# Kernel optimization log

Hardware: AMD Instinct MI355X
Metric: run time of the kernel (lower is better)

Reference implementation:

```python
import jax, jax.numpy as jnp
import numpy as np

L, H, C, HS, E, K, V, BS = 2, 12, 768, 64, 8, 2, 32000, 1024
B, T = 2, 1024


def layer_norm(x, s, b):
    mu = x.mean(-1, keepdims=True)
    var = ((x - mu) ** 2).mean(-1, keepdims=True)
    return (x - mu) / jnp.sqrt(var + 1e-5) * s + b


def setup_inputs() -> dict:
    key = jax.random.key(0)
    ks = jax.random.split(key, 16)
    def n(k, shape, s=0.02):
        return jax.random.normal(k, shape, dtype=jnp.float32) * s
    return {
        'idx': jax.random.randint(ks[0], (B, T), 0, V),
        'targets': jax.random.randint(ks[1], (B, T), 0, V),
        'tok_emb': n(ks[2], (V, C)),
        'pos_emb': n(ks[3], (BS, C)),
        'ln1_s': jnp.ones((L, C), jnp.float32), 'ln1_b': jnp.zeros((L, C), jnp.float32),
        'wq': n(ks[4], (L, H, C, HS)), 'wk': n(ks[5], (L, H, C, HS)), 'wv': n(ks[6], (L, H, C, HS)),
        'wo': n(ks[7], (L, C, C)), 'bo': jnp.zeros((L, C), jnp.float32),
        'ln2_s': jnp.ones((L, C), jnp.float32), 'ln2_b': jnp.zeros((L, C), jnp.float32),
        'gate_w': n(ks[8], (L, E, C)),
        'w1': n(ks[9], (L, E, 4 * C, C)), 'b1': jnp.zeros((L, E, 4 * C), jnp.float32),
        'w2': n(ks[10], (L, E, C, 4 * C)), 'b2': jnp.zeros((L, E, C), jnp.float32),
        'lm_w': n(ks[11], (V, C)), 'lm_b': jnp.zeros((V,), jnp.float32),
    }


def reference(idx, targets, tok_emb, pos_emb, ln1_s, ln1_b, wq, wk, wv, wo, bo,
              ln2_s, ln2_b, gate_w, w1, b1, w2, b2, lm_w, lm_b):
    Bsz, Tn = idx.shape
    x = tok_emb[idx] + pos_emb[:Tn]                       # [B,T,C]
    mask = jnp.tril(jnp.ones((Tn, Tn), bool))
    for l in range(L):
        # causal multi-head attention (per-head projections, scale = n_embed**-0.5 as in source)
        h = layer_norm(x, ln1_s[l], ln1_b[l])
        q = jnp.einsum('btc,hcd->bhtd', h, wq[l])
        k = jnp.einsum('btc,hcd->bhtd', h, wk[l])
        v = jnp.einsum('btc,hcd->bhtd', h, wv[l])
        att = jnp.einsum('bhtd,bhsd->bhts', q, k) * (C ** -0.5)
        att = jax.nn.softmax(jnp.where(mask, att, -jnp.inf), axis=-1)
        o = jnp.einsum('bhts,bhsd->bhtd', att, v)
        o = o.transpose(0, 2, 1, 3).reshape(Bsz, Tn, C)   # concat heads
        x = x + jnp.einsum('btc,oc->bto', o, wo[l]) + bo[l]
        # MoE FFN: top-k routing, softmax over selected gate logits
        h2 = layer_norm(x, ln2_s[l], ln2_b[l]).reshape(-1, C)     # [N,C]
        gl = jnp.einsum('tc,ec->te', h2, gate_w[l])               # [N,E]
        wts, sel = jax.lax.top_k(gl, K)
        wts = jax.nn.softmax(wts, axis=-1)
        comb = jnp.einsum('tk,tke->te', wts, jax.nn.one_hot(sel, E, dtype=wts.dtype))
        hid = jax.nn.relu(jnp.einsum('tc,efc->etf', h2, w1[l]) + b1[l][:, None, :])
        y = jnp.einsum('etf,ecf->etc', hid, w2[l]) + b2[l][:, None, :]
        moe = jnp.einsum('te,etc->tc', comb, y)                   # dispatch-weighted combine
        x = x + moe.reshape(Bsz, Tn, C)
    logits = jnp.einsum('btc,vc->btv', x, lm_w) + lm_b
    lf = logits.reshape(-1, V)
    tf = targets.reshape(-1)
    loss = -jnp.take_along_axis(jax.nn.log_softmax(lf, axis=-1), tf[:, None], axis=1).mean()
    return lf, loss
```

## Files before the change

kernel.cpp:

```cpp
#include <hip/hip_runtime.h>
#include <hip/hip_bf16.h>

#define LCNT 2
#define HCNT 12
#define CDIM 768
#define HSD  64
#define ECNT 8
#define VOC  32000
#define BB   2
#define TT   1024
#define NTOK 2048
#define FF   3072
#define QKVLD 2304
#define TOTCAP 5120

typedef __attribute__((ext_vector_type(8))) short bf16x8;
typedef __attribute__((ext_vector_type(4))) float f32x4;

__device__ __forceinline__ float wave_sum(float v) {
    #pragma unroll
    for (int off = 32; off; off >>= 1) v += __shfl_xor(v, off);
    return v;
}
__device__ __forceinline__ float wave_max(float v) {
    #pragma unroll
    for (int off = 32; off; off >>= 1) v = fmaxf(v, __shfl_xor(v, off));
    return v;
}
__device__ __forceinline__ unsigned short f2bf(float f) {
    unsigned int u = __float_as_uint(f);
    unsigned int r = (u + 0x7FFFu + ((u >> 16) & 1u)) >> 16;
    return (unsigned short)r;
}
__device__ __forceinline__ float bf2f(unsigned short h) {
    return __uint_as_float((unsigned int)h << 16);
}
__device__ __forceinline__ void split2(float a, unsigned short& h, unsigned short& l) {
    h = f2bf(a);
    l = f2bf(a - bf2f(h));
}
__device__ __forceinline__ ushort4 cvt4(float4 v) {
    ushort4 r;
    r.x = f2bf(v.x); r.y = f2bf(v.y); r.z = f2bf(v.z); r.w = f2bf(v.w);
    return r;
}

__global__ __launch_bounds__(256)
void embed_kernel(const int* __restrict__ idx, const float* __restrict__ tok,
                  const float* __restrict__ pos, float* __restrict__ x)
{
    int i = blockIdx.x * 256 + threadIdx.x;
    int c = i % CDIM;
    int n = i / CDIM;
    int t = n % TT;
    x[i] = tok[(size_t)idx[n] * CDIM + c] + pos[(size_t)t * CDIM + c];
}

__global__ __launch_bounds__(256)
void repack_kernel(const float* __restrict__ wq, const float* __restrict__ wk,
                   const float* __restrict__ wv, float* __restrict__ wp)
{
    int i = blockIdx.x * 256 + threadIdx.x;
    int kk = i % CDIM;
    int n  = (i / CDIM) % CDIM;
    int w3 = (i / (CDIM * CDIM)) % 3;
    int l  = i / (CDIM * CDIM * 3);
    const float* src = (w3 == 0) ? wq : (w3 == 1) ? wk : wv;
    int h = n / HSD, d = n % HSD;
    wp[(((size_t)l * 3 + w3) * CDIM + n) * CDIM + kk] =
        src[((((size_t)l * HCNT + h) * CDIM) + kk) * HSD + d];
}

__global__ __launch_bounds__(256)
void ln_kernel(const float* __restrict__ x, const float* __restrict__ sc,
               const float* __restrict__ bs, float* __restrict__ out)
{
    int row = blockIdx.x;
    const float* xr = x + (size_t)row * CDIM;
    float* orow = out + (size_t)row * CDIM;
    int tid = threadIdx.x;
    float v0 = xr[tid], v1 = xr[tid + 256], v2 = xr[tid + 512];
    float s1 = v0 + v1 + v2;
    float s2 = v0 * v0 + v1 * v1 + v2 * v2;
    s1 = wave_sum(s1);
    s2 = wave_sum(s2);
    __shared__ float r1[4], r2[4];
    int w = tid >> 6, lane = tid & 63;
    if (lane == 0) { r1[w] = s1; r2[w] = s2; }
    __syncthreads();
    float t1 = r1[0] + r1[1] + r1[2] + r1[3];
    float t2 = r2[0] + r2[1] + r2[2] + r2[3];
    float mu = t1 * (1.0f / CDIM);
    float var = t2 * (1.0f / CDIM) - mu * mu;
    float rstd = rsqrtf(var + 1e-5f);
    orow[tid]       = (v0 - mu) * rstd * sc[tid]       + bs[tid];
    orow[tid + 256] = (v1 - mu) * rstd * sc[tid + 256] + bs[tid + 256];
    orow[tid + 512] = (v2 - mu) * rstd * sc[tid + 512] + bs[tid + 512];
}

#define BM 128
#define BN 128
#define BK 32
#define PADK 40

template<int MODE, bool SPLIT, bool SWZ = false>
__global__ __launch_bounds__(256)
void gemm_bf16_kernel(int Kd,
                      const float* __restrict__ A, int lda,
                      const float* __restrict__ B, int ldb,
                      const float* __restrict__ bias,
                      float* __restrict__ out, int ldo,
                      const int* __restrict__ rowmeta,
                      size_t bstride, int biasstride)
{
    __shared__ short Ah[BM * PADK];
    __shared__ short Bh[BN * PADK];
    __shared__ short Al[SPLIT ? BM * PADK : 2];
    __shared__ short Bl[SPLIT ? BN * PADK : 2];

    int bx = blockIdx.x, by = blockIdx.y;
    if constexpr (SWZ) {
        const int nwg = gridDim.x * gridDim.y;
        const int chunk = nwg >> 3;
        const int flat = by * gridDim.x + bx;
        const int newid = (flat & 7) * chunk + (flat >> 3);
        by = newid % gridDim.y;
        bx = newid / gridDim.y;
    }

    int roff = 0;
    if (rowmeta) {
        const int ee = blockIdx.z;
        const int rcnt = rowmeta[2 * ee + 1];
        if ((int)(by * BM) >= rcnt) return;
        roff = rowmeta[2 * ee];
        B += (size_t)ee * bstride;
        if (bias) bias += (size_t)ee * biasstride;
    }

    const int tid = threadIdx.x;
    const int m0 = roff + by * BM;
    const int n0 = bx * BN;
    const int w = tid >> 6, lane = tid & 63;
    const int wr = w >> 1, wc = w & 1;
    const int lrow = lane & 15, lkg = lane >> 4;
    const int srow = tid >> 3, skg = (tid & 7) * 4;

    const float* Ablk = A + (size_t)m0 * lda;
    const float* Bblk = B + (size_t)n0 * ldb;

    float4 pa[4], pb[4];
    #pragma unroll
    for (int p = 0; p < 4; ++p) {
        pa[p] = *(const float4*)(Ablk + (size_t)(p * 32 + srow) * lda + skg);
        pb[p] = *(const float4*)(Bblk + (size_t)(p * 32 + srow) * ldb + skg);
    }

    f32x4 acc[4][4] = {};
    const int nk = Kd / BK;

    for (int t = 0; t < nk; ++t) {
        __syncthreads();
        #pragma unroll
        for (int p = 0; p < 4; ++p) {
            if constexpr (SPLIT) {
                ushort4 h, l;
                split2(pa[p].x, h.x, l.x); split2(pa[p].y, h.y, l.y);
                split2(pa[p].z, h.z, l.z); split2(pa[p].w, h.w, l.w);
                *(ushort4*)(&Ah[(p * 32 + srow) * PADK + skg]) = h;
                *(ushort4*)(&Al[(p * 32 + srow) * PADK + skg]) = l;
                split2(pb[p].x, h.x, l.x); split2(pb[p].y, h.y, l.y);
                split2(pb[p].z, h.z, l.z); split2(pb[p].w, h.w, l.w);
                *(ushort4*)(&Bh[(p * 32 + srow) * PADK + skg]) = h;
                *(ushort4*)(&Bl[(p * 32 + srow) * PADK + skg]) = l;
            } else {
                *(ushort4*)(&Ah[(p * 32 + srow) * PADK + skg]) = cvt4(pa[p]);
                *(ushort4*)(&Bh[(p * 32 + srow) * PADK + skg]) = cvt4(pb[p]);
            }
        }
        __syncthreads();
        if (t + 1 < nk) {
            const int kb = (t + 1) * BK + skg;
            #pragma unroll
            for (int p = 0; p < 4; ++p) {
                pa[p] = *(const float4*)(Ablk + (size_t)(p * 32 + srow) * lda + kb);
                pb[p] = *(const float4*)(Bblk + (size_t)(p * 32 + srow) * ldb + kb);
            }
        }
        bf16x8 afh[4], afl[4];
        #pragma unroll
        for (int i = 0; i < 4; ++i) {
            afh[i] = *(const bf16x8*)(&Ah[(wr * 64 + i * 16 + lrow) * PADK + lkg * 8]);
            if constexpr (SPLIT)
                afl[i] = *(const bf16x8*)(&Al[(wr * 64 + i * 16 + lrow) * PADK + lkg * 8]);
        }
        #pragma unroll
        for (int j = 0; j < 4; ++j) {
            const bf16x8 bh = *(const bf16x8*)(&Bh[(wc * 64 + j * 16 + lrow) * PADK + lkg * 8]);
            if constexpr (SPLIT) {
                const bf16x8 bl = *(const bf16x8*)(&Bl[(wc * 64 + j * 16 + lrow) * PADK + lkg * 8]);
                #pragma unroll
                for (int i = 0; i < 4; ++i) {
                    acc[i][j] = __builtin_amdgcn_mfma_f32_16x16x32_bf16(afh[i], bh, acc[i][j], 0, 0, 0);
                    acc[i][j] = __builtin_amdgcn_mfma_f32_16x16x32_bf16(afl[i], bh, acc[i][j], 0, 0, 0);
                    acc[i][j] = __builtin_amdgcn_mfma_f32_16x16x32_bf16(afh[i], bl, acc[i][j], 0, 0, 0);
                }
            } else {
                #pragma unroll
                for (int i = 0; i < 4; ++i)
                    acc[i][j] = __builtin_amdgcn_mfma_f32_16x16x32_bf16(afh[i], bh, acc[i][j], 0, 0, 0);
            }
        }
    }

    #pragma unroll
    for (int i = 0; i < 4; ++i) {
        #pragma unroll
        for (int r = 0; r < 4; ++r) {
            const int row = m0 + wr * 64 + i * 16 + lkg * 4 + r;
            #pragma unroll
            for (int j = 0; j < 4; ++j) {
                const int col = n0 + wc * 64 + j * 16 + lrow;
                const float bj = bias ? bias[col] : 0.0f;
                const float vres = acc[i][j][r] + bj;
                float* op = out + (size_t)row * ldo + col;
                if (MODE == 0) *op = vres;
                else if (MODE == 1) *op = *op + vres;
                else *op = fmaxf(vres, 0.0f);
            }
        }
    }
}

#define QBLK 64
#define KVBLK 64

__global__ __launch_bounds__(256)
void attn_mfma_kernel(const float* __restrict__ qkv, float* __restrict__ o)
{
    __shared__ short Kh[2][KVBLK][PADK];
    __shared__ short Kl[2][KVBLK][PADK];
    __shared__ short Vh[2][HSD][PADK];
    __shared__ short Vl[2][HSD][PADK];
    __shared__ short Ph[4][2][16][PADK];
    __shared__ short Pl[4][2][16][PADK];

    const int t0 = blockIdx.x * QBLK;
    const int bh = blockIdx.y;
    const int b = bh / HCNT, hh = bh % HCNT;
    const size_t baseq = (size_t)b * TT * QKVLD + (size_t)hh * HSD;
    const size_t obase = (size_t)b * TT * CDIM + (size_t)hh * HSD;
    const float* q = qkv + baseq;
    const float* k = qkv + baseq + CDIM;
    const float* v = qkv + baseq + 2 * CDIM;
    const int tid = threadIdx.x;
    const int w = tid >> 6, lane = tid & 63;
    const int lrow = lane & 15, lkg = lane >> 4;
    const float sscale = rsqrtf((float)CDIM);

    bf16x8 qh[2], ql[2];
    {
        const float* qr = q + (size_t)(t0 + w * 16 + lrow) * QKVLD;
        #pragma unroll
        for (int ks = 0; ks < 2; ++ks) {
            #pragma unroll
            for (int j = 0; j < 8; ++j) {
                unsigned short h, l;
                split2(qr[ks * 32 + lkg * 8 + j], h, l);
                qh[ks][j] = (short)h;
                ql[ks][j] = (short)l;
            }
        }
    }

    f32x4 oacc[4] = {};
    float m_[4], l_[4];
    #pragma unroll
    for (int rr = 0; rr < 4; ++rr) { m_[rr] = -1e30f; l_[rr] = 0.0f; }

    for (int s0 = 0; s0 <= t0 + QBLK - 1; s0 += KVBLK) {
        __syncthreads();
        {
            const int srow = tid >> 3, skg = (tid & 7) * 4;
            #pragma unroll
            for (int p = 0; p < 2; ++p) {
                const float* krow = k + (size_t)(s0 + p * 32 + srow) * QKVLD;
                #pragma unroll
                for (int ks = 0; ks < 2; ++ks) {
                    float4 a = *(const float4*)(krow + ks * 32 + skg);
                    ushort4 h, l;
                    split2(a.x, h.x, l.x); split2(a.y, h.y, l.y);
                    split2(a.z, h.z, l.z); split2(a.w, h.w, l.w);
                    *(ushort4*)(&Kh[ks][p * 32 + srow][skg]) = h;
                    *(ushort4*)(&Kl[ks][p * 32 + srow][skg]) = l;
                }
            }
            const int key = tid & 63, dg = (tid >> 6) * 16;
            const float* vrow = v + (size_t)(s0 + key) * QKVLD + dg;
            const int kst = key >> 5, ko = key & 31;
            #pragma unroll
            for (int dd = 0; dd < 16; dd += 4) {
                float4 a = *(const float4*)(vrow + dd);
                unsigned short h, l;
                split2(a.x, h, l); Vh[kst][dg + dd + 0][ko] = h; Vl[kst][dg + dd + 0][ko] = l;
                split2(a.y, h, l); Vh[kst][dg + dd + 1][ko] = h; Vl[kst][dg + dd + 1][ko] = l;
                split2(a.z, h, l); Vh[kst][dg + dd + 2][ko] = h; Vl[kst][dg + dd + 2][ko] = l;
                split2(a.w, h, l); Vh[kst][dg + dd + 3][ko] = h; Vl[kst][dg + dd + 3][ko] = l;
            }
        }
        __syncthreads();

        f32x4 sacc[4] = {};
        #pragma unroll
        for (int j = 0; j < 4; ++j) {
            #pragma unroll
            for (int ks = 0; ks < 2; ++ks) {
                const bf16x8 bh = *(const bf16x8*)(&Kh[ks][j * 16 + lrow][lkg * 8]);
                const bf16x8 bl = *(const bf16x8*)(&Kl[ks][j * 16 + lrow][lkg * 8]);
                sacc[j] = __builtin_amdgcn_mfma_f32_16x16x32_bf16(qh[ks], bh, sacc[j], 0, 0, 0);
                sacc[j] = __builtin_amdgcn_mfma_f32_16x16x32_bf16(ql[ks], bh, sacc[j], 0, 0, 0);
                sacc[j] = __builtin_amdgcn_mfma_f32_16x16x32_bf16(qh[ks], bl, sacc[j], 0, 0, 0);
            }
        }

        #pragma unroll
        for (int rr = 0; rr < 4; ++rr) {
            const int qi = t0 + w * 16 + lkg * 4 + rr;
            float pv[4];
            float mx = -1e30f;
            #pragma unroll
            for (int j = 0; j < 4; ++j) {
                float s = sacc[j][rr] * sscale;
                if (s0 + j * 16 + lrow > qi) s = -1e30f;
                pv[j] = s;
                mx = fmaxf(mx, s);
            }
            #pragma unroll
            for (int off = 1; off < 16; off <<= 1) mx = fmaxf(mx, __shfl_xor(mx, off));
            const float mnew = fmaxf(m_[rr], mx);
            const float corr = __expf(m_[rr] - mnew);
            float ps = 0.0f;
            #pragma unroll
            for (int j = 0; j < 4; ++j) { pv[j] = __expf(pv[j] - mnew); ps += pv[j]; }
            #pragma unroll
            for (int off = 1; off < 16; off <<= 1) ps += __shfl_xor(ps, off);
            l_[rr] = l_[rr] * corr + ps;
            m_[rr] = mnew;
            #pragma unroll
            for (int jd = 0; jd < 4; ++jd) oacc[jd][rr] *= corr;
            #pragma unroll
            for (int j = 0; j < 4; ++j) {
                unsigned short h, l;
                split2(pv[j], h, l);
                const int key = j * 16 + lrow;
                Ph[w][key >> 5][lkg * 4 + rr][key & 31] = h;
                Pl[w][key >> 5][lkg * 4 + rr][key & 31] = l;
            }
        }

        #pragma unroll
        for (int ks = 0; ks < 2; ++ks) {
            const bf16x8 ah = *(const bf16x8*)(&Ph[w][ks][lrow][lkg * 8]);
            const bf16x8 al = *(const bf16x8*)(&Pl[w][ks][lrow][lkg * 8]);
            #pragma unroll
            for (int jd = 0; jd < 4; ++jd) {
                const bf16x8 bh = *(const bf16x8*)(&Vh[ks][jd * 16 + lrow][lkg * 8]);
                const bf16x8 bl = *(const bf16x8*)(&Vl[ks][jd * 16 + lrow][lkg * 8]);
                oacc[jd] = __builtin_amdgcn_mfma_f32_16x16x32_bf16(ah, bh, oacc[jd], 0, 0, 0);
                oacc[jd] = __builtin_amdgcn_mfma_f32_16x16x32_bf16(al, bh, oacc[jd], 0, 0, 0);
                oacc[jd] = __builtin_amdgcn_mfma_f32_16x16x32_bf16(ah, bl, oacc[jd], 0, 0, 0);
            }
        }
    }

    #pragma unroll
    for (int rr = 0; rr < 4; ++rr) {
        const int qi = t0 + w * 16 + lkg * 4 + rr;
        const float invl = 1.0f / l_[rr];
        float* orow = o + obase + (size_t)qi * CDIM;
        #pragma unroll
        for (int jd = 0; jd < 4; ++jd)
            orow[jd * 16 + lrow] = oacc[jd][rr] * invl;
    }
}

__global__ __launch_bounds__(256)
void gate_kernel(const float* __restrict__ h2, const float* __restrict__ gw,
                 int2* __restrict__ sel, float2* __restrict__ wts)
{
    __shared__ float gws[ECNT * CDIM];
    int tid = threadIdx.x;
    for (int i = tid; i < ECNT * CDIM; i += 256) gws[i] = gw[i];
    __syncthreads();
    int t = blockIdx.x * 256 + tid;
    const float* hr = h2 + (size_t)t * CDIM;
    float g[ECNT] = {};
    for (int c = 0; c < CDIM; ++c) {
        float hv = hr[c];
        #pragma unroll
        for (int e = 0; e < ECNT; ++e) g[e] = fmaf(hv, gws[e * CDIM + c], g[e]);
    }
    int e0 = 0; float g0 = g[0];
    #pragma unroll
    for (int e = 1; e < ECNT; ++e) if (g[e] > g0) { g0 = g[e]; e0 = e; }
    int e1 = -1; float g1 = -1e30f;
    #pragma unroll
    for (int e = 0; e < ECNT; ++e) if (e != e0 && g[e] > g1) { g1 = g[e]; e1 = e; }
    float z = __expf(g1 - g0);
    float w0 = 1.0f / (1.0f + z);
    sel[t] = make_int2(e0, e1);
    wts[t] = make_float2(w0, 1.0f - w0);
}

__global__ __launch_bounds__(256)
void route_kernel(const int2* __restrict__ sel, int* __restrict__ perm,
                  int* __restrict__ tokpos, int* __restrict__ meta)
{
    __shared__ int cnt[ECNT], off[ECNT], cur[ECNT];
    const int tid = threadIdx.x;
    if (tid < ECNT) cnt[tid] = 0;
    __syncthreads();
    for (int t = tid; t < NTOK; t += 256) {
        atomicAdd(&cnt[sel[t].x], 1);
        atomicAdd(&cnt[sel[t].y], 1);
    }
    __syncthreads();
    if (tid == 0) {
        int run = 0;
        for (int e = 0; e < ECNT; ++e) {
            off[e] = run; cur[e] = 0;
            int pc = (cnt[e] + BM - 1) / BM * BM;
            meta[2 * e] = run; meta[2 * e + 1] = pc;
            run += pc;
        }
    }
    __syncthreads();
    for (int p = tid; p < TOTCAP; p += 256) perm[p] = 0;
    __syncthreads();
    for (int t = tid; t < NTOK; t += 256) {
        int2 s = sel[t];
        int p0 = atomicAdd(&cur[s.x], 1); perm[off[s.x] + p0] = t; tokpos[2 * t]     = off[s.x] + p0;
        int p1 = atomicAdd(&cur[s.y], 1); perm[off[s.y] + p1] = t; tokpos[2 * t + 1] = off[s.y] + p1;
    }
}

__global__ __launch_bounds__(256)
void gather_kernel(const float* __restrict__ h2, const int* __restrict__ perm,
                   float* __restrict__ xg)
{
    int i = blockIdx.x * 256 + threadIdx.x;
    int c = i % CDIM, p = i / CDIM;
    xg[i] = h2[(size_t)perm[p] * CDIM + c];
}

__global__ __launch_bounds__(256)
void combine_kernel(const float* __restrict__ y, const int* __restrict__ tokpos,
                    const float2* __restrict__ wts, float* __restrict__ x)
{
    int i = blockIdx.x * 256 + threadIdx.x;
    int c = i % CDIM, t = i / CDIM;
    float2 wv = wts[t];
    x[i] += wv.x * y[(size_t)tokpos[2 * t] * CDIM + c]
          + wv.y * y[(size_t)tokpos[2 * t + 1] * CDIM + c];
}

__global__ __launch_bounds__(256)
void loss_row_kernel(const float* __restrict__ logits, const int* __restrict__ tgt,
                     float* __restrict__ lrow)
{
    int row = blockIdx.x;
    const float* lr = logits + (size_t)row * VOC;
    int tid = threadIdx.x, w = tid >> 6, lane = tid & 63;
    __shared__ float red[4];
    float mx = -1e30f;
    for (int i = tid; i < VOC; i += 256) mx = fmaxf(mx, lr[i]);
    mx = wave_max(mx);
    if (lane == 0) red[w] = mx;
    __syncthreads();
    mx = fmaxf(fmaxf(red[0], red[1]), fmaxf(red[2], red[3]));
    __syncthreads();
    float se = 0.0f;
    for (int i = tid; i < VOC; i += 256) se += expf(lr[i] - mx);
    se = wave_sum(se);
    if (lane == 0) red[w] = se;
    __syncthreads();
    if (tid == 0) {
        float lse = mx + logf(red[0] + red[1] + red[2] + red[3]);
        lrow[row] = lse - lr[tgt[row]];
    }
}

__global__ __launch_bounds__(256)
void loss_reduce_kernel(const float* __restrict__ lrow, float* __restrict__ out)
{
    int tid = threadIdx.x, w = tid >> 6, lane = tid & 63;
    float s = 0.0f;
    for (int i = tid; i < NTOK; i += 256) s += lrow[i];
    s = wave_sum(s);
    __shared__ float red[4];
    if (lane == 0) red[w] = s;
    __syncthreads();
    if (tid == 0) out[0] = (red[0] + red[1] + red[2] + red[3]) * (1.0f / NTOK);
}

extern "C" void kernel_launch(void* const* d_in, const int* in_sizes, int n_in,
                              void* d_out, int out_size, void* d_ws, size_t ws_size,
                              hipStream_t stream)
{
    const int*   idx     = (const int*)d_in[0];
    const int*   targets = (const int*)d_in[1];
    const float* tok_emb = (const float*)d_in[2];
    const float* pos_emb = (const float*)d_in[3];
    const float* ln1_s   = (const float*)d_in[4];
    const float* ln1_b   = (const float*)d_in[5];
    const float* wq      = (const float*)d_in[6];
    const float* wk      = (const float*)d_in[7];
    const float* wv      = (const float*)d_in[8];
    const float* wo      = (const float*)d_in[9];
    const float* bo      = (const float*)d_in[10];
    const float* ln2_s   = (const float*)d_in[11];
    const float* ln2_b   = (const float*)d_in[12];
    const float* gate_w  = (const float*)d_in[13];
    const float* w1      = (const float*)d_in[14];
    const float* b1      = (const float*)d_in[15];
    const float* w2      = (const float*)d_in[16];
    const float* b2      = (const float*)d_in[17];
    const float* lm_w    = (const float*)d_in[18];
    const float* lm_b    = (const float*)d_in[19];
    float* out = (float*)d_out;

    float* ws   = (float*)d_ws;
    float* wp   = ws;
    float* x    = wp   + (size_t)3 * LCNT * CDIM * CDIM;
    float* hbuf = x    + (size_t)NTOK * CDIM;
    float* qkv  = hbuf + (size_t)NTOK * CDIM;
    float* xg   = qkv  + (size_t)NTOK * QKVLD;
    float* hid  = xg   + (size_t)TOTCAP * CDIM;
    float* lrow = hid  + (size_t)TOTCAP * FF;
    float2* wts = (float2*)(lrow + NTOK);
    int2*  sel  = (int2*)(wts + NTOK);
    int*   perm = (int*)(sel + NTOK);
    int*  tokpos= perm + TOTCAP;
    int*   meta = tokpos + 2 * NTOK;

    dim3 blk(256);

    repack_kernel<<<(3 * LCNT * CDIM * CDIM) / 256, blk, 0, stream>>>(wq, wk, wv, wp);
    embed_kernel<<<(NTOK * CDIM) / 256, blk, 0, stream>>>(idx, tok_emb, pos_emb, x);

    for (int l = 0; l < LCNT; ++l) {
        ln_kernel<<<NTOK, blk, 0, stream>>>(x, ln1_s + (size_t)l * CDIM, ln1_b + (size_t)l * CDIM, hbuf);

        gemm_bf16_kernel<0, true><<<dim3(QKVLD / BN, NTOK / BM), blk, 0, stream>>>(
            CDIM, hbuf, CDIM, wp + (size_t)l * 3 * CDIM * CDIM, CDIM,
            nullptr, qkv, QKVLD, nullptr, 0, 0);

        attn_mfma_kernel<<<dim3(TT / QBLK, BB * HCNT), blk, 0, stream>>>(qkv, hbuf);

        gemm_bf16_kernel<1, true><<<dim3(CDIM / BN, NTOK / BM), blk, 0, stream>>>(
            CDIM, hbuf, CDIM, wo + (size_t)l * CDIM * CDIM, CDIM,
            bo + (size_t)l * CDIM, x, CDIM, nullptr, 0, 0);

        float* h2 = qkv;
        float* ybuf = qkv;
        ln_kernel<<<NTOK, blk, 0, stream>>>(x, ln2_s + (size_t)l * CDIM, ln2_b + (size_t)l * CDIM, h2);
        gate_kernel<<<NTOK / 256, blk, 0, stream>>>(h2, gate_w + (size_t)l * ECNT * CDIM, sel, wts);
        route_kernel<<<1, blk, 0, stream>>>(sel, perm, tokpos, meta);
        gather_kernel<<<(TOTCAP * CDIM) / 256, blk, 0, stream>>>(h2, perm, xg);

        const float* w1l = w1 + (size_t)l * ECNT * FF * CDIM;
        const float* b1l = b1 + (size_t)l * ECNT * FF;
        const float* w2l = w2 + (size_t)l * ECNT * CDIM * FF;
        const float* b2l = b2 + (size_t)l * ECNT * CDIM;
        if (l == 0) {
            gemm_bf16_kernel<2, true><<<dim3(FF / BN, NTOK / BM, ECNT), blk, 0, stream>>>(
                CDIM, xg, CDIM, w1l, CDIM, b1l, hid, FF, meta, (size_t)FF * CDIM, FF);
            gemm_bf16_kernel<0, true><<<dim3(CDIM / BN, NTOK / BM, ECNT), blk, 0, stream>>>(
                FF, hid, FF, w2l, FF, b2l, ybuf, CDIM, meta, (size_t)CDIM * FF, CDIM);
        } else {
            gemm_bf16_kernel<2, false><<<dim3(FF / BN, NTOK / BM, ECNT), blk, 0, stream>>>(
                CDIM, xg, CDIM, w1l, CDIM, b1l, hid, FF, meta, (size_t)FF * CDIM, FF);
            gemm_bf16_kernel<0, false><<<dim3(CDIM / BN, NTOK / BM, ECNT), blk, 0, stream>>>(
                FF, hid, FF, w2l, FF, b2l, ybuf, CDIM, meta, (size_t)CDIM * FF, CDIM);
        }
        combine_kernel<<<(NTOK * CDIM) / 256, blk, 0, stream>>>(ybuf, tokpos, wts, x);
    }

    gemm_bf16_kernel<0, false, true><<<dim3(VOC / BN, NTOK / BM), blk, 0, stream>>>(
        CDIM, x, CDIM, lm_w, CDIM, lm_b, out, VOC, nullptr, 0, 0);

    loss_row_kernel<<<NTOK, blk, 0, stream>>>(out, targets, lrow);
    loss_reduce_kernel<<<1, blk, 0, stream>>>(lrow, out + (size_t)NTOK * VOC);
}
```

Baseline: 1.508 ms.

## Use bf16 activations and pre-converted weights for layer-1 MoE and LM-head GEMMs

Adds a GEMM variant that reads bf16 A operands, optionally bf16 B, and can write bf16 output. The second-layer MoE FFN now gathers directly into bf16 and stores the hidden activations as bf16. The LM head first converts lm_w and x to bf16 in separate kernels so the GEMM loads half the bytes. The MoE grid's y dimension grows from NTOK/BM to TOTCAP/BM so that experts receiving more than 2048 tokens are fully covered. This cuts memory traffic and in-loop conversions, at the cost of extra conversion passes over the 32000x768 weight every call and lower precision in the intermediates.

Measured after the change: 1.437 ms. -4.7%, faster.

```diff
diff --git a/kernel.cpp b/kernel.cpp
--- a/kernel.cpp
+++ b/kernel.cpp
@@ -46,6 +46,15 @@
 }
 
 __global__ __launch_bounds__(256)
+void cvt_bf16_kernel(const float* __restrict__ in, unsigned short* __restrict__ out, int n4)
+{
+    for (int i = blockIdx.x * 256 + threadIdx.x; i < n4; i += gridDim.x * 256) {
+        float4 v = reinterpret_cast<const float4*>(in)[i];
+        reinterpret_cast<ushort4*>(out)[i] = cvt4(v);
+    }
+}
+
+__global__ __launch_bounds__(256)
 void embed_kernel(const int* __restrict__ idx, const float* __restrict__ tok,
                   const float* __restrict__ pos, float* __restrict__ x)
 {
@@ -103,7 +112,7 @@
 #define BK 32
 #define PADK 40
 
-template<int MODE, bool SPLIT, bool SWZ = false>
+template<int MODE, bool SPLIT>
 __global__ __launch_bounds__(256)
 void gemm_bf16_kernel(int Kd,
                       const float* __restrict__ A, int lda,
@@ -118,29 +127,19 @@
     __shared__ short Al[SPLIT ? BM * PADK : 2];
     __shared__ short Bl[SPLIT ? BN * PADK : 2];
 
-    int bx = blockIdx.x, by = blockIdx.y;
-    if constexpr (SWZ) {
-        const int nwg = gridDim.x * gridDim.y;
-        const int chunk = nwg >> 3;
-        const int flat = by * gridDim.x + bx;
-        const int newid = (flat & 7) * chunk + (flat >> 3);
-        by = newid % gridDim.y;
-        bx = newid / gridDim.y;
-    }
-
     int roff = 0;
     if (rowmeta) {
         const int ee = blockIdx.z;
         const int rcnt = rowmeta[2 * ee + 1];
-        if ((int)(by * BM) >= rcnt) return;
+        if ((int)(blockIdx.y * BM) >= rcnt) return;
         roff = rowmeta[2 * ee];
         B += (size_t)ee * bstride;
         if (bias) bias += (size_t)ee * biasstride;
     }
 
     const int tid = threadIdx.x;
-    const int m0 = roff + by * BM;
-    const int n0 = bx * BN;
+    const int m0 = roff + blockIdx.y * BM;
+    const int n0 = blockIdx.x * BN;
     const int w = tid >> 6, lane = tid & 63;
     const int wr = w >> 1, wc = w & 1;
     const int lrow = lane & 15, lkg = lane >> 4;
@@ -232,6 +231,117 @@
     }
 }
 
+template<int MODE, bool SWZ, bool OUTBF, bool BBF>
+__global__ __launch_bounds__(256)
+void gemm_fastw_kernel(int Kd,
+                       const unsigned short* __restrict__ A, int lda,
+                       const void* __restrict__ Bv, int ldb,
+                       const float* __restrict__ bias,
+                       void* __restrict__ outv, int ldo,
+                       const int* __restrict__ rowmeta,
+                       size_t bstride, int biasstride)
+{
+    __shared__ short Ah[BM * PADK];
+    __shared__ short Bh[BN * PADK];
+
+    int bx = blockIdx.x, by = blockIdx.y;
+    if constexpr (SWZ) {
+        const int nwg = gridDim.x * gridDim.y;
+        const int chunk = nwg >> 3;
+        const int flat = by * gridDim.x + bx;
+        const int newid = (flat & 7) * chunk + (flat >> 3);
+        by = newid % gridDim.y;
+        bx = newid / gridDim.y;
+    }
+
+    const float* Bf = (const float*)Bv;
+    const unsigned short* Bb = (const unsigned short*)Bv;
+    float* outf = (float*)outv;
+    unsigned short* outb = (unsigned short*)outv;
+
+    int roff = 0;
+    if (rowmeta) {
+        const int ee = blockIdx.z;
+        const int rcnt = rowmeta[2 * ee + 1];
+        if ((int)(by * BM) >= rcnt) return;
+        roff = rowmeta[2 * ee];
+        if (BBF) Bb += (size_t)ee * bstride; else Bf += (size_t)ee * bstride;
+        if (bias) bias += (size_t)ee * biasstride;
+    }
+
+    const int tid = threadIdx.x;
+    const int m0 = roff + by * BM;
+    const int n0 = bx * BN;
+    const int w = tid >> 6, lane = tid & 63;
+    const int wr = w >> 1, wc = w & 1;
+    const int lrow = lane & 15, lkg = lane >> 4;
+    const int srow = tid >> 3, skg = (tid & 7) * 4;
+
+    const unsigned short* Ablk = A + (size_t)m0 * lda;
+    const float* Bfblk = Bf + (size_t)n0 * ldb;
+    const unsigned short* Bbblk = Bb + (size_t)n0 * ldb;
+
+    ushort4 pa[4];
+    ushort4 pbb[4];
+    float4  pbf[4];
+    #pragma unroll
+    for (int p = 0; p < 4; ++p) {
+        pa[p] = *(const ushort4*)(Ablk + (size_t)(p * 32 + srow) * lda + skg);
+        if constexpr (BBF) pbb[p] = *(const ushort4*)(Bbblk + (size_t)(p * 32 + srow) * ldb + skg);
+        else               pbf[p] = *(const float4*)(Bfblk + (size_t)(p * 32 + srow) * ldb + skg);
+    }
+
+    f32x4 acc[4][4] = {};
+    const int nk = Kd / BK;
+
+    for (int t = 0; t < nk; ++t) {
+        __syncthreads();
+        #pragma unroll
+        for (int p = 0; p < 4; ++p) {
+            *(ushort4*)(&Ah[(p * 32 + srow) * PADK + skg]) = pa[p];
+            *(ushort4*)(&Bh[(p * 32 + srow) * PADK + skg]) = BBF ? pbb[p] : cvt4(pbf[p]);
+        }
+        __syncthreads();
+        if (t + 1 < nk) {
+            const int kb = (t + 1) * BK + skg;
+            #pragma unroll
+            for (int p = 0; p < 4; ++p) {
+                pa[p] = *(const ushort4*)(Ablk + (size_t)(p * 32 + srow) * lda + kb);
+                if constexpr (BBF) pbb[p] = *(const ushort4*)(Bbblk + (size_t)(p * 32 + srow) * ldb + kb);
+                else               pbf[p] = *(const float4*)(Bfblk + (size_t)(p * 32 + srow) * ldb + kb);
+            }
+        }
+        bf16x8 af[4];
+        #pragma unroll
+        for (int i = 0; i < 4; ++i)
+            af[i] = *(const bf16x8*)(&Ah[(wr * 64 + i * 16 + lrow) * PADK + lkg * 8]);
+        #pragma unroll
+        for (int j = 0; j < 4; ++j) {
+            const bf16x8 bh = *(const bf16x8*)(&Bh[(wc * 64 + j * 16 + lrow) * PADK + lkg * 8]);
+            #pragma unroll
+            for (int i = 0; i < 4; ++i)
+                acc[i][j] = __builtin_amdgcn_mfma_f32_16x16x32_bf16(af[i], bh, acc[i][j], 0, 0, 0);
+        }
+    }
+
+    #pragma unroll
+    for (int i = 0; i < 4; ++i) {
+        #pragma unroll
+        for (int r = 0; r < 4; ++r) {
+            const int row = m0 + wr * 64 + i * 16 + lkg * 4 + r;
+            #pragma unroll
+            for (int j = 0; j < 4; ++j) {
+                const int col = n0 + wc * 64 + j * 16 + lrow;
+                const float bj = bias ? bias[col] : 0.0f;
+                float vres = acc[i][j][r] + bj;
+                if (MODE == 2) vres = fmaxf(vres, 0.0f);
+                if constexpr (OUTBF) outb[(size_t)row * ldo + col] = f2bf(vres);
+                else                 outf[(size_t)row * ldo + col] = vres;
+            }
+        }
+    }
+}
+
 #define QBLK 64
 #define KVBLK 64
 
@@ -451,6 +561,15 @@
     int i = blockIdx.x * 256 + threadIdx.x;
     int c = i % CDIM, p = i / CDIM;
     xg[i] = h2[(size_t)perm[p] * CDIM + c];
+}
+
+__global__ __launch_bounds__(256)
+void gather_bf16_kernel(const float* __restrict__ h2, const int* __restrict__ perm,
+                        unsigned short* __restrict__ xg)
+{
+    int i = blockIdx.x * 256 + threadIdx.x;
+    int c = i % CDIM, p = i / CDIM;
+    xg[i] = f2bf(h2[(size_t)perm[p] * CDIM + c]);
 }
 
 __global__ __launch_bounds__(256)
@@ -542,6 +661,11 @@
     int*   perm = (int*)(sel + NTOK);
     int*  tokpos= perm + TOTCAP;
     int*   meta = tokpos + 2 * NTOK;
+    unsigned short* x_bf = (unsigned short*)(meta + 16);
+
+    unsigned short* xg_bf  = (unsigned short*)xg;
+    unsigned short* hid_bf = (unsigned short*)hid;
+    unsigned short* lmw_bf = (unsigned short*)hid;
 
     dim3 blk(256);
 
@@ -566,28 +690,32 @@
         ln_kernel<<<NTOK, blk, 0, stream>>>(x, ln2_s + (size_t)l * CDIM, ln2_b + (size_t)l * CDIM, h2);
         gate_kernel<<<NTOK / 256, blk, 0, stream>>>(h2, gate_w + (size_t)l * ECNT * CDIM, sel, wts);
         route_kernel<<<1, blk, 0, stream>>>(sel, perm, tokpos, meta);
-        gather_kernel<<<(TOTCAP * CDIM) / 256, blk, 0, stream>>>(h2, perm, xg);
 
         const float* w1l = w1 + (size_t)l * ECNT * FF * CDIM;
         const float* b1l = b1 + (size_t)l * ECNT * FF;
         const float* w2l = w2 + (size_t)l * ECNT * CDIM * FF;
         const float* b2l = b2 + (size_t)l * ECNT * CDIM;
         if (l == 0) {
-            gemm_bf16_kernel<2, true><<<dim3(FF / BN, NTOK / BM, ECNT), blk, 0, stream>>>(
+            gather_kernel<<<(TOTCAP * CDIM) / 256, blk, 0, stream>>>(h2, perm, xg);
+            gemm_bf16_kernel<2, true><<<dim3(FF / BN, TOTCAP / BM, ECNT), blk, 0, stream>>>(
                 CDIM, xg, CDIM, w1l, CDIM, b1l, hid, FF, meta, (size_t)FF * CDIM, FF);
-            gemm_bf16_kernel<0, true><<<dim3(CDIM / BN, NTOK / BM, ECNT), blk, 0, stream>>>(
+            gemm_bf16_kernel<0, true><<<dim3(CDIM / BN, TOTCAP / BM, ECNT), blk, 0, stream>>>(
                 FF, hid, FF, w2l, FF, b2l, ybuf, CDIM, meta, (size_t)CDIM * FF, CDIM);
         } else {
-            gemm_bf16_kernel<2, false><<<dim3(FF / BN, NTOK / BM, ECNT), blk, 0, stream>>>(
-                CDIM, xg, CDIM, w1l, CDIM, b1l, hid, FF, meta, (size_t)FF * CDIM, FF);
-            gemm_bf16_kernel<0, false><<<dim3(CDIM / BN, NTOK / BM, ECNT), blk, 0, stream>>>(
-                FF, hid, FF, w2l, FF, b2l, ybuf, CDIM, meta, (size_t)CDIM * FF, CDIM);
+            gather_bf16_kernel<<<(TOTCAP * CDIM) / 256, blk, 0, stream>>>(h2, perm, xg_bf);
+            gemm_fastw_kernel<2, false, true, false><<<dim3(FF / BN, TOTCAP / BM, ECNT), blk, 0, stream>>>(
+                CDIM, xg_bf, CDIM, w1l, CDIM, b1l, hid_bf, FF, meta, (size_t)FF * CDIM, FF);
+            gemm_fastw_kernel<0, false, false, false><<<dim3(CDIM / BN, TOTCAP / BM, ECNT), blk, 0, stream>>>(
+                FF, hid_bf, FF, w2l, FF, b2l, ybuf, CDIM, meta, (size_t)CDIM * FF, CDIM);
         }
         combine_kernel<<<(NTOK * CDIM) / 256, blk, 0, stream>>>(ybuf, tokpos, wts, x);
     }
 
-    gemm_bf16_kernel<0, false, true><<<dim3(VOC / BN, NTOK / BM), blk, 0, stream>>>(
-        CDIM, x, CDIM, lm_w, CDIM, lm_b, out, VOC, nullptr, 0, 0);
+    cvt_bf16_kernel<<<2048, blk, 0, stream>>>(lm_w, lmw_bf, VOC * CDIM / 4);
+    cvt_bf16_kernel<<<512, blk, 0, stream>>>(x, x_bf, NTOK * CDIM / 4);
+
+    gemm_fastw_kernel<0, true, false, true><<<dim3(VOC / BN, NTOK / BM), blk, 0, stream>>>(
+        CDIM, x_bf, CDIM, lmw_bf, CDIM, lm_b, out, VOC, nullptr, 0, 0);
 
     loss_row_kernel<<<NTOK, blk, 0, stream>>>(out, targets, lrow);
     loss_reduce_kernel<<<1, blk, 0, stream>>>(lrow, out + (size_t)NTOK * VOC);
```
